# Kernel optimization log

Measured on AMD Instinct MI355X. Metric: run time of the kernel, lower is better.

Reference implementation:

```python
import jax, jax.numpy as jnp
import numpy as np

D_MODEL = 1024
N_HEAD = 16
D_K = D_MODEL // N_HEAD
SEQ_LEN = 2048
BATCH = 2
NEG = -1e8


def setup_inputs() -> dict:
    key = jax.random.key(0)
    ks = jax.random.split(key, 8)
    scale = 1.0 / np.sqrt(D_MODEL)
    inp = {
        "input": jax.random.normal(ks[0], (BATCH, SEQ_LEN, D_MODEL), dtype=jnp.float32),
        "mask": jax.random.randint(ks[1], (BATCH, SEQ_LEN), 0, 2) == 1,  # True = masked
        "Wq": jax.random.uniform(ks[2], (D_MODEL, D_MODEL), jnp.float32, -scale, scale),
        "bq": jax.random.uniform(ks[3], (D_MODEL,), jnp.float32, -scale, scale),
        "Wk": jax.random.uniform(ks[4], (D_MODEL, D_MODEL), jnp.float32, -scale, scale),
        "bk": jax.random.uniform(ks[5], (D_MODEL,), jnp.float32, -scale, scale),
        "Wv": jax.random.uniform(ks[6], (D_MODEL, D_MODEL), jnp.float32, -scale, scale),
        "bv": jax.random.uniform(ks[7], (D_MODEL,), jnp.float32, -scale, scale),
    }
    return inp


def reference(input, mask, Wq, bq, Wk, bk, Wv, bv):
    B, S, D = input.shape
    # nn.Linear: y = x @ W^T + b
    def split_heads(x):
        return x.reshape(B, S, N_HEAD, D_K).transpose(0, 2, 1, 3)  # [B,H,S,d_k]

    Q = split_heads(input @ Wq.T + bq)
    K = split_heads(input @ Wk.T + bk)
    V = split_heads(input @ Wv.T + bv)

    scores = jnp.einsum('bhqd,bhkd->bhqk', Q, K) / jnp.sqrt(jnp.float32(D_K))
    # mask [B,S] broadcast over heads and query positions (key mask)
    scores = jnp.where(mask[:, None, None, :], NEG, scores)
    attn = jax.nn.softmax(scores, axis=-1)
    out = jnp.einsum('bhqk,bhkd->bhqd', attn, V)  # [B,H,S,d_k]
    return out.transpose(0, 2, 1, 3).reshape(B, S, D)
```

## Files before the change

kernel.cpp:

```cpp
#include <hip/hip_runtime.h>
#include <hip/hip_bf16.h>
#include <math.h>

#define D_MODEL 1024
#define NH 16
#define DK 64
#define SEQ 2048
#define BATCH 2
#define MTOT (BATCH * SEQ)

typedef unsigned short u16;
typedef unsigned int u32;
typedef short bf16x8 __attribute__((ext_vector_type(8)));
typedef short bf16x4 __attribute__((ext_vector_type(4)));
typedef float f32x4 __attribute__((ext_vector_type(4)));

static constexpr float NEGV2 = -1e8f * 1.44269504089f;
static constexpr float SCL2  = 0.125f * 1.44269504089f;

__device__ __forceinline__ u16 f2bf(float f) {
    union { float f; u32 u; } v; v.f = f;
    u32 r = v.u + 0x7FFFu + ((v.u >> 16) & 1u);
    return (u16)(r >> 16);
}

__device__ __forceinline__ float fexp2(float x) {
#if __has_builtin(__builtin_amdgcn_exp2f)
    return __builtin_amdgcn_exp2f(x);
#else
    return __expf(x * 0.69314718056f);
#endif
}

__device__ __forceinline__ u32 pack2(float lo, float hi) {
    union { __hip_bfloat162 h; u32 u; } cv;
    cv.h = __float22bfloat162_rn(float2{lo, hi});
    return cv.u;
}

__device__ __forceinline__ f32x4 mfma16(bf16x4 a, bf16x4 b, f32x4 c) {
#if __has_builtin(__builtin_amdgcn_mfma_f32_16x16x16_bf16)
    return __builtin_amdgcn_mfma_f32_16x16x16_bf16(a, b, c, 0, 0, 0);
#else
    return __builtin_amdgcn_mfma_f32_16x16x16bf16_1k(a, b, c, 0, 0, 0);
#endif
}

__device__ __forceinline__ void stage16(const u16* g, u16* lds_per_lane) {
#if __has_builtin(__builtin_amdgcn_global_load_lds)
    __builtin_amdgcn_global_load_lds((const __attribute__((address_space(1))) u32*)g,
                                     (__attribute__((address_space(3))) u32*)lds_per_lane,
                                     16, 0, 0);
#else
    *(uint4*)lds_per_lane = *(const uint4*)g;
#endif
}

__global__ __launch_bounds__(256) void convert_bf16(
    const float* __restrict__ X, const float* __restrict__ Wq,
    const float* __restrict__ Wk, const float* __restrict__ Wv,
    const int* __restrict__ mask,
    u16* __restrict__ Xb, u16* __restrict__ Wb, float* __restrict__ madsg)
{
    const int NX = MTOT * D_MODEL / 4;
    const int NW = D_MODEL * D_MODEL / 4;
    const int NM = MTOT / 4;
    int i = blockIdx.x * 256 + threadIdx.x;
    if (i >= NX + 3 * NW + NM) return;
    if (i >= NX + 3 * NW) {
        int j = i - NX - 3 * NW;
        int4 mi = ((const int4*)mask)[j];
        float4 o;
        o.x = mi.x ? NEGV2 : 0.0f; o.y = mi.y ? NEGV2 : 0.0f;
        o.z = mi.z ? NEGV2 : 0.0f; o.w = mi.w ? NEGV2 : 0.0f;
        ((float4*)madsg)[j] = o;
        return;
    }
    float4 v; u16* dst;
    if (i < NX)             { v = ((const float4*)X )[i];            dst = Xb + (size_t)i * 4; }
    else if (i < NX + NW)   { v = ((const float4*)Wq)[i - NX];       dst = Wb + (size_t)(i - NX) * 4; }
    else if (i < NX + 2*NW) { v = ((const float4*)Wk)[i - NX - NW];  dst = Wb + (size_t)NW * 4 + (size_t)(i - NX - NW) * 4; }
    else                    { v = ((const float4*)Wv)[i - NX - 2*NW];dst = Wb + (size_t)NW * 8 + (size_t)(i - NX - 2*NW) * 4; }
    ushort4 o;
    o.x = f2bf(v.x); o.y = f2bf(v.y); o.z = f2bf(v.z); o.w = f2bf(v.w);
    *(ushort4*)dst = o;
}

__global__ __launch_bounds__(256, 2) void proj_mfma(
    const u16* __restrict__ Xb, const u16* __restrict__ Wb,
    const float* __restrict__ bq, const float* __restrict__ bk, const float* __restrict__ bv,
    u16* __restrict__ Qb, u16* __restrict__ Kb, u16* __restrict__ Vb)
{
    __shared__ u16 As[128 * 32];
    __shared__ u16 Bs[128 * 32];

    const int id = blockIdx.x + 32 * blockIdx.y + 256 * blockIdx.z;
    const int swz = (id & 7) * 96 + (id >> 3);
    const int xm = swz & 31;
    const int yn = (swz >> 5) & 7;
    const int zi = swz >> 8;

    const u16* __restrict__ W = Wb + (size_t)zi * D_MODEL * D_MODEL;
    const float* __restrict__ bias = zi == 0 ? bq : (zi == 1 ? bk : bv);
    u16* __restrict__ Out = zi == 0 ? Qb : (zi == 1 ? Kb : Vb);

    const int m0 = xm * 128, n0 = yn * 128;
    const int tid = threadIdx.x, lane = tid & 63, w = tid >> 6;
    const int quad = lane >> 4, l15 = lane & 15;
    const int wr = w >> 1, wc = w & 1;

    f32x4 acc[4][4];
#pragma unroll
    for (int i = 0; i < 4; i++)
#pragma unroll
        for (int j = 0; j < 4; j++) acc[i][j] = (f32x4)0.0f;

    const int srow = 32 * w + (lane >> 2);
    const int scol = (lane & 3) * 8;

    for (int k0 = 0; k0 < D_MODEL; k0 += 32) {
#pragma unroll
        for (int t = 0; t < 2; t++) {
            stage16(Xb + (size_t)(m0 + srow + 16 * t) * D_MODEL + k0 + scol,
                    &As[(32 * w + 16 * t) * 32 + lane * 8]);
            stage16(W + (size_t)(n0 + srow + 16 * t) * D_MODEL + k0 + scol,
                    &Bs[(32 * w + 16 * t) * 32 + lane * 8]);
        }
        __syncthreads();
        bf16x8 af[4], bfr[4];
#pragma unroll
        for (int i = 0; i < 4; i++)
            af[i] = *(const bf16x8*)&As[(wr * 64 + i * 16 + l15) * 32 + quad * 8];
#pragma unroll
        for (int j = 0; j < 4; j++)
            bfr[j] = *(const bf16x8*)&Bs[(wc * 64 + j * 16 + l15) * 32 + quad * 8];
#pragma unroll
        for (int i = 0; i < 4; i++)
#pragma unroll
            for (int j = 0; j < 4; j++)
                acc[i][j] = __builtin_amdgcn_mfma_f32_16x16x32_bf16(af[i], bfr[j], acc[i][j], 0, 0, 0);
        __syncthreads();
    }

    float bj[4];
#pragma unroll
    for (int j = 0; j < 4; j++) bj[j] = bias[n0 + wc * 64 + j * 16 + l15];
#pragma unroll
    for (int i = 0; i < 4; i++) {
#pragma unroll
        for (int j = 0; j < 4; j++) {
#pragma unroll
            for (int r = 0; r < 4; r++) {
                int m = m0 + wr * 64 + i * 16 + quad * 4 + r;
                int n = n0 + wc * 64 + j * 16 + l15;
                int b = m >> 11, s = m & (SEQ - 1);
                int h = n >> 6, d = n & 63;
                Out[(((size_t)b * NH + h) * SEQ + s) * DK + d] = f2bf(acc[i][j][r] + bj[j]);
            }
        }
    }
}

__global__ __launch_bounds__(128, 2) void attn_mfma(
    const u16* __restrict__ Qg, const u16* __restrict__ Kg, const u16* __restrict__ Vg,
    const float* __restrict__ madsg, float* __restrict__ out)
{
    constexpr int PADK = 72, PADV = 72;
    __shared__ u16 Ks[2][64 * PADK];
    __shared__ u16 Vt[2][64 * PADV];

    const int qt0 = blockIdx.x, h = blockIdx.y, b = blockIdx.z;
    const int tid = threadIdx.x, lane = tid & 63, w = tid >> 6;
    const int quad = lane >> 4, l15 = lane & 15;
    const size_t bh = (size_t)b * NH + h;
    const u16* __restrict__ Qp = Qg + (bh * SEQ + qt0 * 64) * DK;
    const u16* __restrict__ Kp = Kg + bh * SEQ * DK;
    const u16* __restrict__ Vp = Vg + bh * SEQ * DK;
    const float* __restrict__ mp = madsg + b * SEQ;

    const int q0 = w * 32;
    bf16x8 qf[2][2];
#pragma unroll
    for (int qt = 0; qt < 2; qt++)
#pragma unroll
        for (int half = 0; half < 2; half++)
            qf[qt][half] = *(const bf16x8*)(Qp + (size_t)(q0 + qt * 16 + l15) * DK + half * 32 + quad * 8);

    const int skey = tid & 63, sdk = (tid >> 6) * 32;
    const int vkp2 = (tid & 31) * 2, vd0 = (tid >> 5) * 16;

    {
        const u16* kr = Kp + (size_t)skey * DK + sdk;
#pragma unroll
        for (int j = 0; j < 4; j++)
            *(bf16x8*)&Ks[0][skey * PADK + sdk + 8 * j] = *(const bf16x8*)(kr + 8 * j);
        const u16* vr = Vp + (size_t)vkp2 * DK + vd0;
        bf16x8 v0a = *(const bf16x8*)vr,        v0b = *(const bf16x8*)(vr + 8);
        bf16x8 v1a = *(const bf16x8*)(vr + DK), v1b = *(const bf16x8*)(vr + DK + 8);
#pragma unroll
        for (int i = 0; i < 8; i++) {
            *(u32*)&Vt[0][(vd0 + i) * PADV + vkp2]     = (u32)(u16)v0a[i] | ((u32)(u16)v1a[i] << 16);
            *(u32*)&Vt[0][(vd0 + 8 + i) * PADV + vkp2] = (u32)(u16)v0b[i] | ((u32)(u16)v1b[i] << 16);
        }
    }
    __syncthreads();

    f32x4 O[4][2];
    f32x4 sacc[2];
#pragma unroll
    for (int dt = 0; dt < 4; dt++)
#pragma unroll
        for (int qt = 0; qt < 2; qt++) O[dt][qt] = (f32x4)0.0f;
    sacc[0] = (f32x4)0.0f; sacc[1] = (f32x4)0.0f;

    for (int kt = 0; kt < SEQ / 64; kt++) {
        const int bb = kt & 1;
        bf16x8 nk[4], nv0a, nv0b, nv1a, nv1b;
        if (kt < SEQ / 64 - 1) {
            const u16* kr = Kp + (size_t)((kt + 1) * 64 + skey) * DK + sdk;
#pragma unroll
            for (int j = 0; j < 4; j++) nk[j] = *(const bf16x8*)(kr + 8 * j);
            const u16* vr = Vp + (size_t)((kt + 1) * 64 + vkp2) * DK + vd0;
            nv0a = *(const bf16x8*)vr;        nv0b = *(const bf16x8*)(vr + 8);
            nv1a = *(const bf16x8*)(vr + DK); nv1b = *(const bf16x8*)(vr + DK + 8);
        }

        f32x4 St[4][2];
#pragma unroll
        for (int ktl = 0; ktl < 4; ktl++) {
            bf16x8 kf0 = *(const bf16x8*)&Ks[bb][(ktl * 16 + l15) * PADK + quad * 8];
            bf16x8 kf1 = *(const bf16x8*)&Ks[bb][(ktl * 16 + l15) * PADK + 32 + quad * 8];
#pragma unroll
            for (int qt = 0; qt < 2; qt++) {
                f32x4 acc = (f32x4)0.0f;
                acc = __builtin_amdgcn_mfma_f32_16x16x32_bf16(kf0, qf[qt][0], acc, 0, 0, 0);
                acc = __builtin_amdgcn_mfma_f32_16x16x32_bf16(kf1, qf[qt][1], acc, 0, 0, 0);
                St[ktl][qt] = acc;
            }
        }

#pragma unroll
        for (int ktl = 0; ktl < 4; ktl++) {
            f32x4 ma = *(const f32x4*)&mp[kt * 64 + ktl * 16 + quad * 4];
#pragma unroll
            for (int qt = 0; qt < 2; qt++)
#pragma unroll
                for (int r = 0; r < 4; r++) {
                    float p = fexp2(St[ktl][qt][r] * SCL2 + ma[r]);
                    St[ktl][qt][r] = p;
                    sacc[qt][r] += p;
                }
        }

        bf16x4 pf[4][2];
#pragma unroll
        for (int ktl = 0; ktl < 4; ktl++)
#pragma unroll
            for (int qt = 0; qt < 2; qt++) {
                union { u32 u[2]; bf16x4 v; } pu;
                pu.u[0] = pack2(St[ktl][qt][0], St[ktl][qt][1]);
                pu.u[1] = pack2(St[ktl][qt][2], St[ktl][qt][3]);
                pf[ktl][qt] = pu.v;
            }

#pragma unroll
        for (int ktl = 0; ktl < 4; ktl++)
#pragma unroll
            for (int dt = 0; dt < 4; dt++) {
                bf16x4 vf = *(const bf16x4*)&Vt[bb][(dt * 16 + l15) * PADV + ktl * 16 + quad * 4];
#pragma unroll
                for (int qt = 0; qt < 2; qt++)
                    O[dt][qt] = mfma16(vf, pf[ktl][qt], O[dt][qt]);
            }

        if (kt < SEQ / 64 - 1) {
#pragma unroll
            for (int j = 0; j < 4; j++)
                *(bf16x8*)&Ks[bb ^ 1][skey * PADK + sdk + 8 * j] = nk[j];
#pragma unroll
            for (int i = 0; i < 8; i++) {
                *(u32*)&Vt[bb ^ 1][(vd0 + i) * PADV + vkp2]     = (u32)(u16)nv0a[i] | ((u32)(u16)nv1a[i] << 16);
                *(u32*)&Vt[bb ^ 1][(vd0 + 8 + i) * PADV + vkp2] = (u32)(u16)nv0b[i] | ((u32)(u16)nv1b[i] << 16);
            }
        }
        __syncthreads();
    }

    float inv[2];
#pragma unroll
    for (int qt = 0; qt < 2; qt++) {
        float s = (sacc[qt][0] + sacc[qt][1]) + (sacc[qt][2] + sacc[qt][3]);
        s += __shfl_xor(s, 16);
        s += __shfl_xor(s, 32);
        inv[qt] = 1.0f / s;
    }
#pragma unroll
    for (int qt = 0; qt < 2; qt++) {
        int q = qt0 * 64 + q0 + qt * 16 + l15;
        float* op = out + ((size_t)b * SEQ + q) * D_MODEL + h * DK;
#pragma unroll
        for (int dt = 0; dt < 4; dt++)
#pragma unroll
            for (int r = 0; r < 4; r++)
                op[dt * 16 + quad * 4 + r] = O[dt][qt][r] * inv[qt];
    }
}

extern "C" void kernel_launch(void* const* d_in, const int* in_sizes, int n_in,
                              void* d_out, int out_size, void* d_ws, size_t ws_size,
                              hipStream_t stream)
{
    const float* X  = (const float*)d_in[0];
    const int* mask = (const int*)d_in[1];
    const float* Wq = (const float*)d_in[2];
    const float* bq = (const float*)d_in[3];
    const float* Wk = (const float*)d_in[4];
    const float* bk = (const float*)d_in[5];
    const float* Wv = (const float*)d_in[6];
    const float* bv = (const float*)d_in[7];
    float* out = (float*)d_out;

    u16* Xb = (u16*)d_ws;
    u16* Wb = Xb + (size_t)MTOT * D_MODEL;
    u16* Qb = Wb + (size_t)3 * D_MODEL * D_MODEL;
    u16* Kb = Qb + (size_t)BATCH * NH * SEQ * DK;
    u16* Vb = Kb + (size_t)BATCH * NH * SEQ * DK;
    float* madsg = (float*)(Vb + (size_t)BATCH * NH * SEQ * DK);

    const int ncvt = (MTOT * D_MODEL + 3 * D_MODEL * D_MODEL + MTOT) / 4;
    convert_bf16<<<(ncvt + 255) / 256, 256, 0, stream>>>(X, Wq, Wk, Wv, mask, Xb, Wb, madsg);
    proj_mfma<<<dim3(MTOT / 128, D_MODEL / 128, 3), 256, 0, stream>>>(Xb, Wb, bq, bk, bv, Qb, Kb, Vb);
    attn_mfma<<<dim3(SEQ / 64, NH, BATCH), 128, 0, stream>>>(Qb, Kb, Vb, madsg, out);
}
```

Measured before the change: 188.5 us.

## Split key range across two wave groups in 512-thread attention blocks

The attention kernel now processes 128 queries per block with 512 threads. Two 256-thread groups each sweep half of the key sequence, and their partial outputs and row sums are combined through shared memory at the end. Each K/V tile loaded to LDS is now shared by four waves instead of two, and the key loop is half as long per wave. In exchange, LDS double buffering is replaced by a single buffer guarded by two barriers per tile, and a final cross-group reduction is added.

```diff
diff --git a/kernel.cpp b/kernel.cpp
--- a/kernel.cpp
+++ b/kernel.cpp
@@ -161,24 +161,31 @@
     }
 }
 
-__global__ __launch_bounds__(128, 2) void attn_mfma(
+__global__ __launch_bounds__(512, 4) void attn_mfma(
     const u16* __restrict__ Qg, const u16* __restrict__ Kg, const u16* __restrict__ Vg,
     const float* __restrict__ madsg, float* __restrict__ out)
 {
     constexpr int PADK = 72, PADV = 72;
-    __shared__ u16 Ks[2][64 * PADK];
-    __shared__ u16 Vt[2][64 * PADV];
+    constexpr int HK = SEQ / 2;
+    constexpr int NT = HK / 64;
+    __shared__ u16 smem[2][64 * PADK + 64 * PADV];
 
     const int qt0 = blockIdx.x, h = blockIdx.y, b = blockIdx.z;
-    const int tid = threadIdx.x, lane = tid & 63, w = tid >> 6;
+    const int tid = threadIdx.x, lane = tid & 63;
+    const int wg = (tid >> 6) & 3;
+    const int grp = tid >> 8;
+    const int g = tid & 255;
     const int quad = lane >> 4, l15 = lane & 15;
     const size_t bh = (size_t)b * NH + h;
-    const u16* __restrict__ Qp = Qg + (bh * SEQ + qt0 * 64) * DK;
-    const u16* __restrict__ Kp = Kg + bh * SEQ * DK;
-    const u16* __restrict__ Vp = Vg + bh * SEQ * DK;
-    const float* __restrict__ mp = madsg + b * SEQ;
-
-    const int q0 = w * 32;
+    const u16* __restrict__ Qp = Qg + (bh * SEQ + qt0 * 128) * DK;
+    const u16* __restrict__ Kp = Kg + (bh * SEQ + (size_t)grp * HK) * DK;
+    const u16* __restrict__ Vp = Vg + (bh * SEQ + (size_t)grp * HK) * DK;
+    const float* __restrict__ mp = madsg + b * SEQ + grp * HK;
+
+    u16* __restrict__ KbL = &smem[grp][0];
+    u16* __restrict__ VbL = &smem[grp][64 * PADK];
+
+    const int q0 = wg * 32;
     bf16x8 qf[2][2];
 #pragma unroll
     for (int qt = 0; qt < 2; qt++)
@@ -186,24 +193,16 @@
         for (int half = 0; half < 2; half++)
             qf[qt][half] = *(const bf16x8*)(Qp + (size_t)(q0 + qt * 16 + l15) * DK + half * 32 + quad * 8);
 
-    const int skey = tid & 63, sdk = (tid >> 6) * 32;
-    const int vkp2 = (tid & 31) * 2, vd0 = (tid >> 5) * 16;
-
+    const int skey = g & 63, sdk = (g >> 6) * 16;
+    const int vkp2 = (g & 31) * 2, vd0 = (g >> 5) * 8;
+
+    bf16x8 nk0, nk1, nv0, nv1;
     {
         const u16* kr = Kp + (size_t)skey * DK + sdk;
-#pragma unroll
-        for (int j = 0; j < 4; j++)
-            *(bf16x8*)&Ks[0][skey * PADK + sdk + 8 * j] = *(const bf16x8*)(kr + 8 * j);
+        nk0 = *(const bf16x8*)kr; nk1 = *(const bf16x8*)(kr + 8);
         const u16* vr = Vp + (size_t)vkp2 * DK + vd0;
-        bf16x8 v0a = *(const bf16x8*)vr,        v0b = *(const bf16x8*)(vr + 8);
-        bf16x8 v1a = *(const bf16x8*)(vr + DK), v1b = *(const bf16x8*)(vr + DK + 8);
-#pragma unroll
-        for (int i = 0; i < 8; i++) {
-            *(u32*)&Vt[0][(vd0 + i) * PADV + vkp2]     = (u32)(u16)v0a[i] | ((u32)(u16)v1a[i] << 16);
-            *(u32*)&Vt[0][(vd0 + 8 + i) * PADV + vkp2] = (u32)(u16)v0b[i] | ((u32)(u16)v1b[i] << 16);
-        }
-    }
-    __syncthreads();
+        nv0 = *(const bf16x8*)vr; nv1 = *(const bf16x8*)(vr + DK);
+    }
 
     f32x4 O[4][2];
     f32x4 sacc[2];
@@ -213,23 +212,28 @@
         for (int qt = 0; qt < 2; qt++) O[dt][qt] = (f32x4)0.0f;
     sacc[0] = (f32x4)0.0f; sacc[1] = (f32x4)0.0f;
 
-    for (int kt = 0; kt < SEQ / 64; kt++) {
-        const int bb = kt & 1;
-        bf16x8 nk[4], nv0a, nv0b, nv1a, nv1b;
-        if (kt < SEQ / 64 - 1) {
-            const u16* kr = Kp + (size_t)((kt + 1) * 64 + skey) * DK + sdk;
-#pragma unroll
-            for (int j = 0; j < 4; j++) nk[j] = *(const bf16x8*)(kr + 8 * j);
-            const u16* vr = Vp + (size_t)((kt + 1) * 64 + vkp2) * DK + vd0;
-            nv0a = *(const bf16x8*)vr;        nv0b = *(const bf16x8*)(vr + 8);
-            nv1a = *(const bf16x8*)(vr + DK); nv1b = *(const bf16x8*)(vr + DK + 8);
+    for (int t = 0; t < NT; t++) {
+        __syncthreads();
+        {
+            u16* kd = &KbL[skey * PADK + sdk];
+            *(bf16x8*)kd = nk0; *(bf16x8*)(kd + 8) = nk1;
+#pragma unroll
+            for (int i = 0; i < 8; i++)
+                *(u32*)&VbL[(vd0 + i) * PADV + vkp2] = (u32)(u16)nv0[i] | ((u32)(u16)nv1[i] << 16);
+        }
+        __syncthreads();
+        if (t < NT - 1) {
+            const u16* kr = Kp + (size_t)((t + 1) * 64 + skey) * DK + sdk;
+            nk0 = *(const bf16x8*)kr; nk1 = *(const bf16x8*)(kr + 8);
+            const u16* vr = Vp + (size_t)((t + 1) * 64 + vkp2) * DK + vd0;
+            nv0 = *(const bf16x8*)vr; nv1 = *(const bf16x8*)(vr + DK);
         }
 
         f32x4 St[4][2];
 #pragma unroll
         for (int ktl = 0; ktl < 4; ktl++) {
-            bf16x8 kf0 = *(const bf16x8*)&Ks[bb][(ktl * 16 + l15) * PADK + quad * 8];
-            bf16x8 kf1 = *(const bf16x8*)&Ks[bb][(ktl * 16 + l15) * PADK + 32 + quad * 8];
+            bf16x8 kf0 = *(const bf16x8*)&KbL[(ktl * 16 + l15) * PADK + quad * 8];
+            bf16x8 kf1 = *(const bf16x8*)&KbL[(ktl * 16 + l15) * PADK + 32 + quad * 8];
 #pragma unroll
             for (int qt = 0; qt < 2; qt++) {
                 f32x4 acc = (f32x4)0.0f;
@@ -241,7 +245,7 @@
 
 #pragma unroll
         for (int ktl = 0; ktl < 4; ktl++) {
-            f32x4 ma = *(const f32x4*)&mp[kt * 64 + ktl * 16 + quad * 4];
+            f32x4 ma = *(const f32x4*)&mp[t * 64 + ktl * 16 + quad * 4];
 #pragma unroll
             for (int qt = 0; qt < 2; qt++)
 #pragma unroll
@@ -267,42 +271,54 @@
         for (int ktl = 0; ktl < 4; ktl++)
 #pragma unroll
             for (int dt = 0; dt < 4; dt++) {
-                bf16x4 vf = *(const bf16x4*)&Vt[bb][(dt * 16 + l15) * PADV + ktl * 16 + quad * 4];
+                bf16x4 vf = *(const bf16x4*)&VbL[(dt * 16 + l15) * PADV + ktl * 16 + quad * 4];
 #pragma unroll
                 for (int qt = 0; qt < 2; qt++)
                     O[dt][qt] = mfma16(vf, pf[ktl][qt], O[dt][qt]);
             }
-
-        if (kt < SEQ / 64 - 1) {
-#pragma unroll
-            for (int j = 0; j < 4; j++)
-                *(bf16x8*)&Ks[bb ^ 1][skey * PADK + sdk + 8 * j] = nk[j];
-#pragma unroll
-            for (int i = 0; i < 8; i++) {
-                *(u32*)&Vt[bb ^ 1][(vd0 + i) * PADV + vkp2]     = (u32)(u16)nv0a[i] | ((u32)(u16)nv1a[i] << 16);
-                *(u32*)&Vt[bb ^ 1][(vd0 + 8 + i) * PADV + vkp2] = (u32)(u16)nv0b[i] | ((u32)(u16)nv1b[i] << 16);
-            }
-        }
-        __syncthreads();
-    }
-
-    float inv[2];
+    }
+
+    float sred[2];
 #pragma unroll
     for (int qt = 0; qt < 2; qt++) {
         float s = (sacc[qt][0] + sacc[qt][1]) + (sacc[qt][2] + sacc[qt][3]);
         s += __shfl_xor(s, 16);
         s += __shfl_xor(s, 32);
-        inv[qt] = 1.0f / s;
-    }
-#pragma unroll
-    for (int qt = 0; qt < 2; qt++) {
-        int q = qt0 * 64 + q0 + qt * 16 + l15;
-        float* op = out + ((size_t)b * SEQ + q) * D_MODEL + h * DK;
-#pragma unroll
-        for (int dt = 0; dt < 4; dt++)
-#pragma unroll
-            for (int r = 0; r < 4; r++)
-                op[dt * 16 + quad * 4 + r] = O[dt][qt][r] * inv[qt];
+        sred[qt] = s;
+    }
+
+    __syncthreads();
+    float* fsm = (float*)&smem[0][0];
+    if (grp == 1) {
+#pragma unroll
+        for (int qt = 0; qt < 2; qt++)
+#pragma unroll
+            for (int dt = 0; dt < 4; dt++)
+#pragma unroll
+                for (int r = 0; r < 4; r++)
+                    fsm[(qt * 16 + dt * 4 + r) * 256 + wg * 64 + lane] = O[dt][qt][r];
+#pragma unroll
+        for (int qt = 0; qt < 2; qt++)
+            fsm[8192 + (wg * 16 + l15) * 2 + qt] = sred[qt];
+    }
+    __syncthreads();
+    if (grp == 0) {
+        float inv[2];
+#pragma unroll
+        for (int qt = 0; qt < 2; qt++)
+            inv[qt] = 1.0f / (sred[qt] + fsm[8192 + (wg * 16 + l15) * 2 + qt]);
+#pragma unroll
+        for (int qt = 0; qt < 2; qt++) {
+            int q = qt0 * 128 + q0 + qt * 16 + l15;
+            float* op = out + ((size_t)b * SEQ + q) * D_MODEL + h * DK;
+#pragma unroll
+            for (int dt = 0; dt < 4; dt++)
+#pragma unroll
+                for (int r = 0; r < 4; r++) {
+                    float v = O[dt][qt][r] + fsm[(qt * 16 + dt * 4 + r) * 256 + wg * 64 + lane];
+                    op[dt * 16 + quad * 4 + r] = v * inv[qt];
+                }
+        }
     }
 }
 
@@ -330,5 +346,5 @@
     const int ncvt = (MTOT * D_MODEL + 3 * D_MODEL * D_MODEL + MTOT) / 4;
     convert_bf16<<<(ncvt + 255) / 256, 256, 0, stream>>>(X, Wq, Wk, Wv, mask, Xb, Wb, madsg);
     proj_mfma<<<dim3(MTOT / 128, D_MODEL / 128, 3), 256, 0, stream>>>(Xb, Wb, bq, bk, bv, Qb, Kb, Vb);
-    attn_mfma<<<dim3(SEQ / 64, NH, BATCH), 128, 0, stream>>>(Qb, Kb, Vb, madsg, out);
-}
+    attn_mfma<<<dim3(SEQ / 128, NH, BATCH), 512, 0, stream>>>(Qb, Kb, Vb, madsg, out);
+}
```

Result: no change. 187.5 us (-0.5%).

## Load K fragments directly into registers and double attention block size

Applied to the files above, without the earlier changes.

K tiles are no longer staged through shared memory. Each wave loads its MFMA K fragments straight from global memory into registers and prefetches the next tile's fragments one iteration ahead. The attention block grows from 2 to 4 waves covering 128 queries, so each V tile in LDS is shared by more waves and the grid halves. This removes LDS traffic for K but makes every wave fetch K redundantly from global/L2 and raises register pressure.

```diff
diff --git a/kernel.cpp b/kernel.cpp
--- a/kernel.cpp
+++ b/kernel.cpp
@@ -161,19 +161,18 @@
     }
 }
 
-__global__ __launch_bounds__(128, 2) void attn_mfma(
+__global__ __launch_bounds__(256, 2) void attn_mfma(
     const u16* __restrict__ Qg, const u16* __restrict__ Kg, const u16* __restrict__ Vg,
     const float* __restrict__ madsg, float* __restrict__ out)
 {
-    constexpr int PADK = 72, PADV = 72;
-    __shared__ u16 Ks[2][64 * PADK];
+    constexpr int PADV = 72;
     __shared__ u16 Vt[2][64 * PADV];
 
     const int qt0 = blockIdx.x, h = blockIdx.y, b = blockIdx.z;
     const int tid = threadIdx.x, lane = tid & 63, w = tid >> 6;
     const int quad = lane >> 4, l15 = lane & 15;
     const size_t bh = (size_t)b * NH + h;
-    const u16* __restrict__ Qp = Qg + (bh * SEQ + qt0 * 64) * DK;
+    const u16* __restrict__ Qp = Qg + (bh * SEQ + qt0 * 128) * DK;
     const u16* __restrict__ Kp = Kg + bh * SEQ * DK;
     const u16* __restrict__ Vp = Vg + bh * SEQ * DK;
     const float* __restrict__ mp = madsg + b * SEQ;
@@ -186,22 +185,22 @@
         for (int half = 0; half < 2; half++)
             qf[qt][half] = *(const bf16x8*)(Qp + (size_t)(q0 + qt * 16 + l15) * DK + half * 32 + quad * 8);
 
-    const int skey = tid & 63, sdk = (tid >> 6) * 32;
-    const int vkp2 = (tid & 31) * 2, vd0 = (tid >> 5) * 16;
-
+    const u16* __restrict__ Kf = Kp + (size_t)l15 * DK + quad * 8;
+
+    const int vkp2 = (tid & 31) * 2, vd0 = (tid >> 5) * 8;
+
+    bf16x8 kf[4][2];
+#pragma unroll
+    for (int ktl = 0; ktl < 4; ktl++)
+#pragma unroll
+        for (int half = 0; half < 2; half++)
+            kf[ktl][half] = *(const bf16x8*)(Kf + (size_t)(ktl * 16) * DK + half * 32);
     {
-        const u16* kr = Kp + (size_t)skey * DK + sdk;
-#pragma unroll
-        for (int j = 0; j < 4; j++)
-            *(bf16x8*)&Ks[0][skey * PADK + sdk + 8 * j] = *(const bf16x8*)(kr + 8 * j);
         const u16* vr = Vp + (size_t)vkp2 * DK + vd0;
-        bf16x8 v0a = *(const bf16x8*)vr,        v0b = *(const bf16x8*)(vr + 8);
-        bf16x8 v1a = *(const bf16x8*)(vr + DK), v1b = *(const bf16x8*)(vr + DK + 8);
-#pragma unroll
-        for (int i = 0; i < 8; i++) {
-            *(u32*)&Vt[0][(vd0 + i) * PADV + vkp2]     = (u32)(u16)v0a[i] | ((u32)(u16)v1a[i] << 16);
-            *(u32*)&Vt[0][(vd0 + 8 + i) * PADV + vkp2] = (u32)(u16)v0b[i] | ((u32)(u16)v1b[i] << 16);
-        }
+        bf16x8 v0 = *(const bf16x8*)vr, v1 = *(const bf16x8*)(vr + DK);
+#pragma unroll
+        for (int i = 0; i < 8; i++)
+            *(u32*)&Vt[0][(vd0 + i) * PADV + vkp2] = (u32)(u16)v0[i] | ((u32)(u16)v1[i] << 16);
     }
     __syncthreads();
 
@@ -215,26 +214,26 @@
 
     for (int kt = 0; kt < SEQ / 64; kt++) {
         const int bb = kt & 1;
-        bf16x8 nk[4], nv0a, nv0b, nv1a, nv1b;
+        bf16x8 nv0, nv1, kfn[4][2];
         if (kt < SEQ / 64 - 1) {
-            const u16* kr = Kp + (size_t)((kt + 1) * 64 + skey) * DK + sdk;
-#pragma unroll
-            for (int j = 0; j < 4; j++) nk[j] = *(const bf16x8*)(kr + 8 * j);
             const u16* vr = Vp + (size_t)((kt + 1) * 64 + vkp2) * DK + vd0;
-            nv0a = *(const bf16x8*)vr;        nv0b = *(const bf16x8*)(vr + 8);
-            nv1a = *(const bf16x8*)(vr + DK); nv1b = *(const bf16x8*)(vr + DK + 8);
+            nv0 = *(const bf16x8*)vr; nv1 = *(const bf16x8*)(vr + DK);
+            const u16* kb = Kf + (size_t)((kt + 1) * 64) * DK;
+#pragma unroll
+            for (int ktl = 0; ktl < 4; ktl++)
+#pragma unroll
+                for (int half = 0; half < 2; half++)
+                    kfn[ktl][half] = *(const bf16x8*)(kb + (size_t)(ktl * 16) * DK + half * 32);
         }
 
         f32x4 St[4][2];
 #pragma unroll
         for (int ktl = 0; ktl < 4; ktl++) {
-            bf16x8 kf0 = *(const bf16x8*)&Ks[bb][(ktl * 16 + l15) * PADK + quad * 8];
-            bf16x8 kf1 = *(const bf16x8*)&Ks[bb][(ktl * 16 + l15) * PADK + 32 + quad * 8];
 #pragma unroll
             for (int qt = 0; qt < 2; qt++) {
                 f32x4 acc = (f32x4)0.0f;
-                acc = __builtin_amdgcn_mfma_f32_16x16x32_bf16(kf0, qf[qt][0], acc, 0, 0, 0);
-                acc = __builtin_amdgcn_mfma_f32_16x16x32_bf16(kf1, qf[qt][1], acc, 0, 0, 0);
+                acc = __builtin_amdgcn_mfma_f32_16x16x32_bf16(kf[ktl][0], qf[qt][0], acc, 0, 0, 0);
+                acc = __builtin_amdgcn_mfma_f32_16x16x32_bf16(kf[ktl][1], qf[qt][1], acc, 0, 0, 0);
                 St[ktl][qt] = acc;
             }
         }
@@ -275,13 +274,13 @@
 
         if (kt < SEQ / 64 - 1) {
 #pragma unroll
-            for (int j = 0; j < 4; j++)
-                *(bf16x8*)&Ks[bb ^ 1][skey * PADK + sdk + 8 * j] = nk[j];
-#pragma unroll
-            for (int i = 0; i < 8; i++) {
-                *(u32*)&Vt[bb ^ 1][(vd0 + i) * PADV + vkp2]     = (u32)(u16)nv0a[i] | ((u32)(u16)nv1a[i] << 16);
-                *(u32*)&Vt[bb ^ 1][(vd0 + 8 + i) * PADV + vkp2] = (u32)(u16)nv0b[i] | ((u32)(u16)nv1b[i] << 16);
-            }
+            for (int i = 0; i < 8; i++)
+                *(u32*)&Vt[bb ^ 1][(vd0 + i) * PADV + vkp2] = (u32)(u16)nv0[i] | ((u32)(u16)nv1[i] << 16);
+#pragma unroll
+            for (int ktl = 0; ktl < 4; ktl++)
+#pragma unroll
+                for (int half = 0; half < 2; half++)
+                    kf[ktl][half] = kfn[ktl][half];
         }
         __syncthreads();
     }
@@ -296,7 +295,7 @@
     }
 #pragma unroll
     for (int qt = 0; qt < 2; qt++) {
-        int q = qt0 * 64 + q0 + qt * 16 + l15;
+        int q = qt0 * 128 + q0 + qt * 16 + l15;
         float* op = out + ((size_t)b * SEQ + q) * D_MODEL + h * DK;
 #pragma unroll
         for (int dt = 0; dt < 4; dt++)
@@ -330,5 +329,5 @@
     const int ncvt = (MTOT * D_MODEL + 3 * D_MODEL * D_MODEL + MTOT) / 4;
     convert_bf16<<<(ncvt + 255) / 256, 256, 0, stream>>>(X, Wq, Wk, Wv, mask, Xb, Wb, madsg);
     proj_mfma<<<dim3(MTOT / 128, D_MODEL / 128, 3), 256, 0, stream>>>(Xb, Wb, bq, bk, bv, Qb, Kb, Vb);
-    attn_mfma<<<dim3(SEQ / 64, NH, BATCH), 128, 0, stream>>>(Qb, Kb, Vb, madsg, out);
-}
+    attn_mfma<<<dim3(SEQ / 128, NH, BATCH), 256, 0, stream>>>(Qb, Kb, Vb, madsg, out);
+}
```

New measurement: 218.8 us. 1.16x slower.
